# Kernel tuning notes

Hardware: AMD Instinct MI355X
Metric: run time of the kernel (lower is better)

The kernel has to match this reference:

```python
import jax, jax.numpy as jnp
import numpy as np

D_ATTN = 64

def setup_inputs() -> dict:
    key = jax.random.key(0)
    k1, k2, k3 = jax.random.split(key, 3)
    B, N, d_ffn = 8, 2048, 1536
    x = jax.random.normal(k1, (B, N, d_ffn), dtype=jnp.float32)
    W_qkv = jax.random.normal(k2, (d_ffn, 3 * D_ATTN), dtype=jnp.float32) * (1.0 / np.sqrt(d_ffn))
    b_qkv = jnp.zeros((3 * D_ATTN,), dtype=jnp.float32)
    W_out = jax.random.normal(k3, (D_ATTN, d_ffn // 2), dtype=jnp.float32) * (1.0 / np.sqrt(D_ATTN))
    b_out = jnp.zeros((d_ffn // 2,), dtype=jnp.float32)
    return {"x": x, "W_qkv": W_qkv, "b_qkv": b_qkv, "W_out": W_out, "b_out": b_out}

def reference(x, W_qkv, b_qkv, W_out, b_out):
    # x: [B, N, d_ffn]
    qkv = jnp.einsum('bnd,de->bne', x, W_qkv) + b_qkv  # [B, N, 3*d_attn]
    q, k, v = jnp.split(qkv, 3, axis=-1)               # each [B, N, d_attn]
    scale = 1.0 / jnp.sqrt(jnp.float32(D_ATTN))
    energy = jnp.einsum('bqd,bkd->bqk', q, k) * scale  # [B, N, N]
    attn = jax.nn.softmax(energy, axis=-1)
    out = jnp.einsum('bqk,bkd->bqd', attn, v)          # [B, N, d_attn]
    out = jnp.einsum('bnd,de->bne', out, W_out) + b_out  # [B, N, d_ffn//2]
    return out
```

## Files before the change

kernel.cpp:

```cpp
#include <hip/hip_runtime.h>
#include <hip/hip_bf16.h>


typedef __attribute__((ext_vector_type(8))) short short8;
typedef __attribute__((ext_vector_type(4))) short short4v;
typedef __attribute__((ext_vector_type(4))) float float4v;
typedef __attribute__((ext_vector_type(16))) float float16v;

#define MFMA16(a, b, c) __builtin_amdgcn_mfma_f32_16x16x32_bf16((a), (b), (c), 0, 0, 0)
#define MFMA32(a, b, c) __builtin_amdgcn_mfma_f32_32x32x16_bf16((a), (b), (c), 0, 0, 0)

static __device__ __forceinline__ void plswap(unsigned& a, unsigned& b) {
  asm("v_permlane32_swap_b32 %0, %1" : "+v"(a), "+v"(b));
}

static __device__ __forceinline__ unsigned short f2bf(float x) {
  union { float f; unsigned u; } v; v.f = x;
  return (unsigned short)((v.u + 0x7FFFu + ((v.u >> 16) & 1u)) >> 16);
}
static __device__ __forceinline__ short8 ldg8(const short* p) {
  return *(const short8*)p;
}

__global__ __launch_bounds__(256) void k_prep(
    const float* __restrict__ Wq, const float* __restrict__ Wo,
    short* __restrict__ Wtf, short* __restrict__ WtO) {
  __shared__ float wl[64 * 52];
  __shared__ __align__(16) short tl[64 * 72];
  const int tid = threadIdx.x;
  int id = blockIdx.x;
  if (id < 96) {
    const int kk = id >> 2, w = id & 3;
    const int r = tid >> 2, cq = (tid & 3) * 12;
    const float* sp = Wq + (size_t)(kk * 64 + r) * 192 + w * 48 + cq;
    float4v a = *(const float4v*)(sp);
    float4v b = *(const float4v*)(sp + 4);
    float4v c4 = *(const float4v*)(sp + 8);
    float* dp = wl + r * 52 + cq;
    *(float4v*)(dp) = a; *(float4v*)(dp + 4) = b; *(float4v*)(dp + 8) = c4;
    __syncthreads();
#pragma unroll
    for (int i = 0; i < 2; ++i) {
      const int fid = i * 256 + tid;
      if (fid < 384) {
        const int frag = fid >> 6, lane = fid & 63;
        const int lo = lane & 15, hi = lane >> 4;
        const int c = frag >> 1, ks = frag & 1;
        short8 o;
#pragma unroll
        for (int e = 0; e < 8; ++e)
          o[e] = (short)f2bf(wl[(ks * 32 + hi * 8 + e) * 52 + c * 16 + lo]);
        *(short8*)(Wtf + ((((size_t)kk * 4 + w) * 6 + frag) << 9) + lane * 8) = o;
      }
    }
  } else {
    id -= 96;
    const int r = tid >> 2, cq = (tid & 3) * 16;
    const float* sp = Wo + (size_t)r * 768 + id * 64 + cq;
    float4v v0 = *(const float4v*)(sp);
    float4v v1 = *(const float4v*)(sp + 4);
    float4v v2 = *(const float4v*)(sp + 8);
    float4v v3 = *(const float4v*)(sp + 12);
    short8 s0, s1;
#pragma unroll
    for (int i = 0; i < 4; ++i) {
      s0[i] = (short)f2bf(v0[i]); s0[i + 4] = (short)f2bf(v1[i]);
      s1[i] = (short)f2bf(v2[i]); s1[i + 4] = (short)f2bf(v3[i]);
    }
    *(short8*)(tl + r * 72 + cq) = s0;
    *(short8*)(tl + r * 72 + cq + 8) = s1;
    __syncthreads();
    short8 o0, o1;
#pragma unroll
    for (int j = 0; j < 8; ++j) {
      o0[j] = tl[(cq + j) * 72 + r];
      o1[j] = tl[(cq + 8 + j) * 72 + r];
    }
    short* dp2 = WtO + (size_t)(id * 64 + r) * 64 + cq;
    *(short8*)(dp2) = o0;
    *(short8*)(dp2 + 8) = o1;
  }
}

__global__ __launch_bounds__(256) void k_qkv(
    const float* __restrict__ x, const short* __restrict__ Wtf,
    const float* __restrict__ bq, short* __restrict__ Qf,
    short* __restrict__ Kf, short* __restrict__ Vf) {
  __shared__ __align__(16) short xl[2][32 * 72];
  __shared__ __align__(16) short qbuf[32 * 72], kstg[32 * 72], vstg[32 * 72];
  const int tid = threadIdx.x;
  const int w = tid >> 6, lane = tid & 63, lo = lane & 15, hi = lane >> 4;
  const int m0 = blockIdx.x * 32;
  const float KSC = 0.18033688011112042f;
  const int cb = w * 48;

  float4v acc[2][3];
#pragma unroll
  for (int r = 0; r < 2; ++r)
#pragma unroll
    for (int c = 0; c < 3; ++c) acc[r][c] = (float4v)0.0f;

  const int xr = tid >> 3, xc = (tid & 7) * 8;
  const float* xrow = x + (size_t)(m0 + xr) * 1536 + xc;
  short* xlw0 = &xl[0][xr * 72 + xc];
  short* xlw1 = &xl[1][xr * 72 + xc];

  const short* wbase = Wtf + ((size_t)w * 6) * 512 + lane * 8;

  float4v xv0 = *(const float4v*)(xrow + 0);
  float4v xv1 = *(const float4v*)(xrow + 4);
  short8 bcur[3][2];
#pragma unroll
  for (int c = 0; c < 3; ++c)
#pragma unroll
    for (int ks = 0; ks < 2; ++ks)
      bcur[c][ks] = ldg8(wbase + (c * 2 + ks) * 512);
  {
    short8 s0;
#pragma unroll
    for (int i = 0; i < 4; ++i) { s0[i] = (short)f2bf(xv0[i]); s0[i + 4] = (short)f2bf(xv1[i]); }
    *(short8*)(xlw0) = s0;
  }
  __syncthreads();

  for (int kk = 0; kk < 24; ++kk) {
    const int cur = kk & 1;
    short8 bnxt[3][2];
    if (kk < 23) {
      const int k1 = (kk + 1) * 64;
      xv0 = *(const float4v*)(xrow + k1 + 0);
      xv1 = *(const float4v*)(xrow + k1 + 4);
      const short* wn = wbase + (size_t)(kk + 1) * 12288;
#pragma unroll
      for (int c = 0; c < 3; ++c)
#pragma unroll
        for (int ks = 0; ks < 2; ++ks)
          bnxt[c][ks] = ldg8(wn + (c * 2 + ks) * 512);
    }
    const short* xb = &xl[cur][0];
#pragma unroll
    for (int r = 0; r < 2; ++r) {
      short8 a0 = *(const short8*)(xb + (r * 16 + lo) * 72 + hi * 8);
      short8 a1 = *(const short8*)(xb + (r * 16 + lo) * 72 + 32 + hi * 8);
#pragma unroll
      for (int c = 0; c < 3; ++c) {
        acc[r][c] = MFMA16(a0, bcur[c][0], acc[r][c]);
        acc[r][c] = MFMA16(a1, bcur[c][1], acc[r][c]);
      }
    }
    if (kk < 23) {
      short8 s0;
#pragma unroll
      for (int i = 0; i < 4; ++i) { s0[i] = (short)f2bf(xv0[i]); s0[i + 4] = (short)f2bf(xv1[i]); }
      *(short8*)(cur ? xlw0 : xlw1) = s0;
#pragma unroll
      for (int c = 0; c < 3; ++c) { bcur[c][0] = bnxt[c][0]; bcur[c][1] = bnxt[c][1]; }
    }
    __syncthreads();
  }

  float bb[3];
#pragma unroll
  for (int c = 0; c < 3; ++c) bb[c] = bq[cb + c * 16 + lo];

  const int b = m0 >> 11;
  const int row0 = m0 & 2047;

#pragma unroll
  for (int r = 0; r < 2; ++r)
#pragma unroll
    for (int c = 0; c < 3; ++c) {
      const int colb = cb + c * 16;
      short* buf = (colb < 64) ? qbuf : ((colb < 128) ? kstg : vstg);
      const int d0 = (colb & 63) + lo;
#pragma unroll
      for (int j = 0; j < 4; ++j) {
        float vv = acc[r][c][j] + bb[c];
        if (colb < 64) vv *= KSC;
        buf[(r * 16 + hi * 4 + j) * 72 + d0] = (short)f2bf(vv);
      }
    }
  __syncthreads();

  {
    const int rr = tid >> 3, dq = (tid & 7) * 8;
    const int t32 = row0 >> 5, i = dq >> 4, h = (dq >> 3) & 1;
    const size_t base = ((((size_t)b * 64 + t32) * 4 + i) * 2 + h) * 256 + rr * 8;
    *(short8*)(Qf + base) = *(const short8*)(qbuf + rr * 72 + dq);
    *(short8*)(Kf + base) = *(const short8*)(kstg + rr * 72 + dq);
  }

  {
    const int dr = tid >> 2, kq8 = (tid & 3) * 8;
    short8 o0;
#pragma unroll
    for (int j = 0; j < 8; ++j) o0[j] = vstg[(kq8 + j) * 72 + dr];
    const int kg = row0 >> 5, s = (kq8 >> 4) & 1, h = (kq8 >> 3) & 1;
    const int dc = dr >> 5, c32 = dr & 31;
    short* vp = Vf + ((((((size_t)b * 64 + kg) * 2 + dc) * 2 + s) * 2 + h) * 32 + c32) * 8;
    *(short8*)(vp) = o0;
  }
}

__global__ __launch_bounds__(512) void k_attn(
    const short* __restrict__ Qf, const short* __restrict__ Kf,
    const short* __restrict__ Vf, short* __restrict__ att) {
  __shared__ float Od[8][32][76];
  __shared__ float Ol[8][32];
  const int tid = threadIdx.x;
  const int w = tid >> 6, lane = tid & 63;
  const int c = lane & 31, h = lane >> 5;
  const int b = blockIdx.x >> 6;
  const int qg = blockIdx.x & 63;
  const size_t g0 = (size_t)b * 2048 + qg * 32;

  short8 qf0 = ldg8(Qf + (((size_t)b * 64 + qg) * 4 + 0) * 512 + lane * 8);
  short8 qf1 = ldg8(Qf + (((size_t)b * 64 + qg) * 4 + 1) * 512 + lane * 8);
  short8 qf2 = ldg8(Qf + (((size_t)b * 64 + qg) * 4 + 2) * 512 + lane * 8);
  short8 qf3 = ldg8(Qf + (((size_t)b * 64 + qg) * 4 + 3) * 512 + lane * 8);

  float lp = 0.0f;
  float16v acc0 = (float16v)0.0f;
  float16v acc1 = (float16v)0.0f;

  int kg = w * 8;
  const short* kb = Kf + ((size_t)b * 64) * 2048 + lane * 8;
  const short* vb = Vf + ((size_t)b * 64) * 2048 + lane * 8;

#define ATTN_STEP(K0, K1, K2, K3, V0, V1, V2, V3)                              \
  do {                                                                         \
    float16v sf = (float16v)0.0f;                                              \
    sf = MFMA32(K0, qf0, sf);                                                  \
    sf = MFMA32(K1, qf1, sf);                                                  \
    sf = MFMA32(K2, qf2, sf);                                                  \
    sf = MFMA32(K3, qf3, sf);                                                  \
    unsigned wpk[8];                                                           \
    _Pragma("unroll")                                                          \
    for (int m = 0; m < 8; ++m) {                                              \
      float p0 = __builtin_amdgcn_exp2f(sf[2 * m]);                            \
      float p1 = __builtin_amdgcn_exp2f(sf[2 * m + 1]);                        \
      unsigned u0 = __builtin_bit_cast(unsigned, p0) & 0xFFFF0000u;            \
      unsigned u1 = __builtin_bit_cast(unsigned, p1) & 0xFFFF0000u;            \
      lp += __builtin_bit_cast(float, u0) + __builtin_bit_cast(float, u1);     \
      wpk[m] = (u0 >> 16) | u1;                                                \
    }                                                                          \
    plswap(wpk[0], wpk[2]);                                                    \
    plswap(wpk[1], wpk[3]);                                                    \
    plswap(wpk[4], wpk[6]);                                                    \
    plswap(wpk[5], wpk[7]);                                                    \
    union { unsigned u[4]; short8 s8; } bt0, bt1;                              \
    bt0.u[0] = wpk[0]; bt0.u[1] = wpk[1]; bt0.u[2] = wpk[2]; bt0.u[3] = wpk[3];\
    bt1.u[0] = wpk[4]; bt1.u[1] = wpk[5]; bt1.u[2] = wpk[6]; bt1.u[3] = wpk[7];\
    acc0 = MFMA32(V0, bt0.s8, acc0);                                           \
    acc0 = MFMA32(V1, bt1.s8, acc0);                                           \
    acc1 = MFMA32(V2, bt0.s8, acc1);                                           \
    acc1 = MFMA32(V3, bt1.s8, acc1);                                           \
  } while (0)

  const short* kpA = kb + (size_t)kg * 2048;
  const short* vpA = vb + (size_t)kg * 2048;
  short8 ka0 = ldg8(kpA), ka1 = ldg8(kpA + 512), ka2 = ldg8(kpA + 1024), ka3 = ldg8(kpA + 1536);
  short8 va0 = ldg8(vpA), va1 = ldg8(vpA + 512), va2 = ldg8(vpA + 1024), va3 = ldg8(vpA + 1536);

  for (int t = 0; t < 8; t += 2) {
    const short* kpB = kb + (size_t)(kg + 1) * 2048;
    const short* vpB = vb + (size_t)(kg + 1) * 2048;
    short8 kb0 = ldg8(kpB), kb1 = ldg8(kpB + 512), kb2 = ldg8(kpB + 1024), kb3 = ldg8(kpB + 1536);
    short8 vb0 = ldg8(vpB), vb1 = ldg8(vpB + 512), vb2 = ldg8(vpB + 1024), vb3 = ldg8(vpB + 1536);

    ATTN_STEP(ka0, ka1, ka2, ka3, va0, va1, va2, va3);

    if (t + 2 < 8) {
      const short* kpN = kb + (size_t)(kg + 2) * 2048;
      const short* vpN = vb + (size_t)(kg + 2) * 2048;
      ka0 = ldg8(kpN); ka1 = ldg8(kpN + 512); ka2 = ldg8(kpN + 1024); ka3 = ldg8(kpN + 1536);
      va0 = ldg8(vpN); va1 = ldg8(vpN + 512); va2 = ldg8(vpN + 1024); va3 = ldg8(vpN + 1536);
    }

    ATTN_STEP(kb0, kb1, kb2, kb3, vb0, vb1, vb2, vb3);
    kg += 2;
  }
#undef ATTN_STEP

  lp += __shfl_xor(lp, 32, 64);

#pragma unroll
  for (int g = 0; g < 4; ++g) {
    float4v a0, a1;
#pragma unroll
    for (int r = 0; r < 4; ++r) { a0[r] = acc0[4 * g + r]; a1[r] = acc1[4 * g + r]; }
    *(float4v*)(&Od[w][c][8 * g + 4 * h]) = a0;
    *(float4v*)(&Od[w][c][32 + 8 * g + 4 * h]) = a1;
  }
  if (h == 0) Ol[w][c] = lp;
  __syncthreads();

  {
    const int q = tid >> 4, dq = (tid & 15) * 4;
    float L = 0.0f;
    float4v o = (float4v)0.0f;
#pragma unroll
    for (int w2 = 0; w2 < 8; ++w2) {
      L += Ol[w2][q];
      o += *(const float4v*)(&Od[w2][q][dq]);
    }
    const float inv = 1.0f / L;
    short4v r;
#pragma unroll
    for (int j = 0; j < 4; ++j) r[j] = (short)f2bf(o[j] * inv);
    *(short4v*)(att + (g0 + q) * 64 + dq) = r;
  }
}

__global__ __launch_bounds__(256) void k_out(
    const short* __restrict__ att, const short* __restrict__ WtO,
    const float* __restrict__ bo, float* __restrict__ out) {
  const int tid = threadIdx.x;
  const int w = tid >> 6, lane = tid & 63, lo = lane & 15, hi = lane >> 4;
  const int wc = w * 192;
  const int m0 = blockIdx.x * 32;

  short8 af[2][2];
#pragma unroll
  for (int rf = 0; rf < 2; ++rf) {
    const short* ap = att + (size_t)(m0 + rf * 16 + lo) * 64 + hi * 8;
    af[rf][0] = ldg8(ap);
    af[rf][1] = ldg8(ap + 32);
  }
  float4v acc[2][12];
#pragma unroll
  for (int rf = 0; rf < 2; ++rf)
#pragma unroll
    for (int c = 0; c < 12; ++c) acc[rf][c] = (float4v)0.0f;

#pragma unroll
  for (int c = 0; c < 12; ++c) {
    const short* bp = WtO + (size_t)(wc + c * 16 + lo) * 64 + hi * 8;
    short8 b0 = ldg8(bp);
    short8 b1 = ldg8(bp + 32);
#pragma unroll
    for (int rf = 0; rf < 2; ++rf) {
      acc[rf][c] = MFMA16(af[rf][0], b0, acc[rf][c]);
      acc[rf][c] = MFMA16(af[rf][1], b1, acc[rf][c]);
    }
  }
#pragma unroll
  for (int c = 0; c < 12; ++c) {
    const float bb = bo[wc + c * 16 + lo];
#pragma unroll
    for (int rf = 0; rf < 2; ++rf)
#pragma unroll
      for (int j = 0; j < 4; ++j)
        out[(size_t)(m0 + rf * 16 + hi * 4 + j) * 768 + wc + c * 16 + lo] =
            acc[rf][c][j] + bb;
  }
}

extern "C" void kernel_launch(void* const* d_in, const int* in_sizes, int n_in,
                              void* d_out, int out_size, void* d_ws, size_t ws_size,
                              hipStream_t stream) {
  (void)in_sizes; (void)n_in; (void)out_size; (void)ws_size;
  const float* x  = (const float*)d_in[0];
  const float* Wq = (const float*)d_in[1];
  const float* bq = (const float*)d_in[2];
  const float* Wo = (const float*)d_in[3];
  const float* bo = (const float*)d_in[4];
  float* out = (float*)d_out;

  char* ws = (char*)d_ws;
  short* Qf  = (short*)(ws);
  short* Kf  = (short*)(ws + 2097152);
  short* Vf  = (short*)(ws + 4194304);
  short* att = (short*)(ws + 6291456);
  short* Wtf = (short*)(ws + 8388608);
  short* WtO = (short*)(ws + 8978432);

  k_prep<<<108, 256, 0, stream>>>(Wq, Wo, Wtf, WtO);
  k_qkv<<<512, 256, 0, stream>>>(x, Wtf, bq, Qf, Kf, Vf);
  k_attn<<<512, 512, 0, stream>>>(Qf, Kf, Vf, att);
  k_out<<<512, 256, 0, stream>>>(att, WtO, bo, out);
}
```

Baseline: 61.91 us.

## Fuse output projection into attention kernel and use lighter LDS barriers

Merges the output projection into the attention kernel. Each 512-thread block writes its normalized bf16 attention rows into shared memory, reusing the Od buffer, and its 8 waves each compute 96 output columns with MFMA. This removes a kernel launch and the global round-trip of the attention intermediate. It also replaces __syncthreads in the QKV kernel with an explicit lgkmcnt wait plus s_barrier, which avoids waiting on outstanding global loads at each barrier. The cost is extra epilogue work and register pressure inside the already heavy attention kernel.

```diff
diff --git a/kernel.cpp b/kernel.cpp
--- a/kernel.cpp
+++ b/kernel.cpp
@@ -9,6 +9,8 @@
 
 #define MFMA16(a, b, c) __builtin_amdgcn_mfma_f32_16x16x32_bf16((a), (b), (c), 0, 0, 0)
 #define MFMA32(a, b, c) __builtin_amdgcn_mfma_f32_32x32x16_bf16((a), (b), (c), 0, 0, 0)
+
+#define LDS_BARRIER() asm volatile("s_waitcnt lgkmcnt(0)\n\ts_barrier" ::: "memory")
 
 static __device__ __forceinline__ void plswap(unsigned& a, unsigned& b) {
   asm("v_permlane32_swap_b32 %0, %1" : "+v"(a), "+v"(b));
@@ -121,7 +123,7 @@
     for (int i = 0; i < 4; ++i) { s0[i] = (short)f2bf(xv0[i]); s0[i + 4] = (short)f2bf(xv1[i]); }
     *(short8*)(xlw0) = s0;
   }
-  __syncthreads();
+  LDS_BARRIER();
 
   for (int kk = 0; kk < 24; ++kk) {
     const int cur = kk & 1;
@@ -156,7 +158,7 @@
 #pragma unroll
       for (int c = 0; c < 3; ++c) { bcur[c][0] = bnxt[c][0]; bcur[c][1] = bnxt[c][1]; }
     }
-    __syncthreads();
+    LDS_BARRIER();
   }
 
   float bb[3];
@@ -180,7 +182,7 @@
         buf[(r * 16 + hi * 4 + j) * 72 + d0] = (short)f2bf(vv);
       }
     }
-  __syncthreads();
+  LDS_BARRIER();
 
   {
     const int rr = tid >> 3, dq = (tid & 7) * 8;
@@ -202,17 +204,19 @@
   }
 }
 
-__global__ __launch_bounds__(512) void k_attn(
+__global__ __launch_bounds__(512) void k_attnout(
     const short* __restrict__ Qf, const short* __restrict__ Kf,
-    const short* __restrict__ Vf, short* __restrict__ att) {
-  __shared__ float Od[8][32][76];
+    const short* __restrict__ Vf, const short* __restrict__ WtO,
+    const float* __restrict__ bo, float* __restrict__ out) {
+  __shared__ __align__(16) float Od[8][32][76];
   __shared__ float Ol[8][32];
   const int tid = threadIdx.x;
   const int w = tid >> 6, lane = tid & 63;
   const int c = lane & 31, h = lane >> 5;
+  const int lo = lane & 15, hi = lane >> 4;
   const int b = blockIdx.x >> 6;
   const int qg = blockIdx.x & 63;
-  const size_t g0 = (size_t)b * 2048 + qg * 32;
+  const int m0 = blockIdx.x * 32;
 
   short8 qf0 = ldg8(Qf + (((size_t)b * 64 + qg) * 4 + 0) * 512 + lane * 8);
   short8 qf1 = ldg8(Qf + (((size_t)b * 64 + qg) * 4 + 1) * 512 + lane * 8);
@@ -295,6 +299,7 @@
   if (h == 0) Ol[w][c] = lp;
   __syncthreads();
 
+  short4v attr;
   {
     const int q = tid >> 4, dq = (tid & 15) * 4;
     float L = 0.0f;
@@ -305,54 +310,51 @@
       o += *(const float4v*)(&Od[w2][q][dq]);
     }
     const float inv = 1.0f / L;
-    short4v r;
-#pragma unroll
-    for (int j = 0; j < 4; ++j) r[j] = (short)f2bf(o[j] * inv);
-    *(short4v*)(att + (g0 + q) * 64 + dq) = r;
-  }
-}
-
-__global__ __launch_bounds__(256) void k_out(
-    const short* __restrict__ att, const short* __restrict__ WtO,
-    const float* __restrict__ bo, float* __restrict__ out) {
-  const int tid = threadIdx.x;
-  const int w = tid >> 6, lane = tid & 63, lo = lane & 15, hi = lane >> 4;
-  const int wc = w * 192;
-  const int m0 = blockIdx.x * 32;
-
+#pragma unroll
+    for (int j = 0; j < 4; ++j) attr[j] = (short)f2bf(o[j] * inv);
+  }
+  __syncthreads();
+
+  short* attL = (short*)&Od[0][0][0];
+  {
+    const int q = tid >> 4, dq = (tid & 15) * 4;
+    *(short4v*)(attL + q * 72 + dq) = attr;
+  }
+  LDS_BARRIER();
+
+  const int wc = w * 96;
   short8 af[2][2];
 #pragma unroll
   for (int rf = 0; rf < 2; ++rf) {
-    const short* ap = att + (size_t)(m0 + rf * 16 + lo) * 64 + hi * 8;
-    af[rf][0] = ldg8(ap);
-    af[rf][1] = ldg8(ap + 32);
-  }
-  float4v acc[2][12];
+    af[rf][0] = *(const short8*)(attL + (rf * 16 + lo) * 72 + hi * 8);
+    af[rf][1] = *(const short8*)(attL + (rf * 16 + lo) * 72 + 32 + hi * 8);
+  }
+  float4v oacc[2][6];
 #pragma unroll
   for (int rf = 0; rf < 2; ++rf)
 #pragma unroll
-    for (int c = 0; c < 12; ++c) acc[rf][c] = (float4v)0.0f;
-
-#pragma unroll
-  for (int c = 0; c < 12; ++c) {
-    const short* bp = WtO + (size_t)(wc + c * 16 + lo) * 64 + hi * 8;
+    for (int cc = 0; cc < 6; ++cc) oacc[rf][cc] = (float4v)0.0f;
+
+#pragma unroll
+  for (int cc = 0; cc < 6; ++cc) {
+    const short* bp = WtO + (size_t)(wc + cc * 16 + lo) * 64 + hi * 8;
     short8 b0 = ldg8(bp);
     short8 b1 = ldg8(bp + 32);
 #pragma unroll
     for (int rf = 0; rf < 2; ++rf) {
-      acc[rf][c] = MFMA16(af[rf][0], b0, acc[rf][c]);
-      acc[rf][c] = MFMA16(af[rf][1], b1, acc[rf][c]);
-    }
-  }
-#pragma unroll
-  for (int c = 0; c < 12; ++c) {
-    const float bb = bo[wc + c * 16 + lo];
+      oacc[rf][cc] = MFMA16(af[rf][0], b0, oacc[rf][cc]);
+      oacc[rf][cc] = MFMA16(af[rf][1], b1, oacc[rf][cc]);
+    }
+  }
+#pragma unroll
+  for (int cc = 0; cc < 6; ++cc) {
+    const float bb = bo[wc + cc * 16 + lo];
 #pragma unroll
     for (int rf = 0; rf < 2; ++rf)
 #pragma unroll
       for (int j = 0; j < 4; ++j)
-        out[(size_t)(m0 + rf * 16 + hi * 4 + j) * 768 + wc + c * 16 + lo] =
-            acc[rf][c][j] + bb;
+        out[(size_t)(m0 + rf * 16 + hi * 4 + j) * 768 + wc + cc * 16 + lo] =
+            oacc[rf][cc][j] + bb;
   }
 }
 
@@ -371,12 +373,10 @@
   short* Qf  = (short*)(ws);
   short* Kf  = (short*)(ws + 2097152);
   short* Vf  = (short*)(ws + 4194304);
-  short* att = (short*)(ws + 6291456);
   short* Wtf = (short*)(ws + 8388608);
   short* WtO = (short*)(ws + 8978432);
 
   k_prep<<<108, 256, 0, stream>>>(Wq, Wo, Wtf, WtO);
   k_qkv<<<512, 256, 0, stream>>>(x, Wtf, bq, Qf, Kf, Vf);
-  k_attn<<<512, 512, 0, stream>>>(Qf, Kf, Vf, att);
-  k_out<<<512, 256, 0, stream>>>(att, WtO, bo, out);
-}
+  k_attnout<<<512, 512, 0, stream>>>(Qf, Kf, Vf, WtO, bo, out);
+}
```

Result: faster. 59.97 us (-3.1%).
